# Kernel optimization log

Measured on AMD Instinct MI355X. Metric: run time of the kernel, lower is better.

Reference implementation:

```python
import jax, jax.numpy as jnp
import numpy as np

B, C, H, W = 16, 4, 512, 512


def setup_inputs() -> dict:
    key = jax.random.key(0)
    k_in, k_tg, k_mask = jax.random.split(key, 3)
    inp = jax.random.normal(k_in, (B, C, H, W), dtype=jnp.float32)
    tgt_vals = jax.random.normal(k_tg, (B, C, H, W), dtype=jnp.float32)
    mask = jax.random.randint(k_mask, (B, 1, H, W), 0, 2).astype(jnp.float32)
    target = jnp.concatenate([tgt_vals, mask], axis=1)  # [B, C+1, H, W]
    return {"input": inp, "target": target}


def reference(input, target):
    # mask = target[b, -1]; masked_select broadcasts mask over the C channels,
    # MSELoss means over the C*count selected elements; batches with empty
    # masks contribute 0; each batch contribution is divided by B.
    mask = (target[:, -1] == 1).astype(input.dtype)            # [B, H, W]
    diff2 = jnp.square(input - target[:, :-1])                 # [B, C, H, W]
    sum_b = jnp.einsum("bchw,bhw->b", diff2, mask)             # masked SSE per batch
    cnt_b = mask.sum(axis=(1, 2)) * input.shape[1]             # C * #masked pixels
    per_b = jnp.where(cnt_b > 0, sum_b / jnp.maximum(cnt_b, 1.0), 0.0)
    return per_b.sum() / input.shape[0]
```

## Files before the change

kernel.cpp:

```cpp
#include <hip/hip_runtime.h>


#define BATCH 16
#define CHAN 4
#define HWPIX (512 * 512)
#define BLOCKS_PER_BATCH 64
#define THREADS 256

__global__ __launch_bounds__(THREADS) void masked_mse_partial(
    const float* __restrict__ input,
    const float* __restrict__ target,
    float* __restrict__ ws) {
    const int b   = blockIdx.x / BLOCKS_PER_BATCH;
    const int blk = blockIdx.x % BLOCKS_PER_BATCH;

    const int groups           = HWPIX / 4;
    const int groups_per_block = groups / BLOCKS_PER_BATCH;

    const float* inb = input  + (size_t)b * CHAN * HWPIX;
    const float* tgb = target + (size_t)b * (CHAN + 1) * HWPIX;
    const float4* mask4 = (const float4*)(tgb + (size_t)CHAN * HWPIX);

    float s = 0.f, cnt = 0.f;

    const int g_end = (blk + 1) * groups_per_block;
    for (int g = blk * groups_per_block + threadIdx.x; g < g_end; g += THREADS) {
        float4 m = mask4[g];
        float mx = (m.x == 1.f) ? 1.f : 0.f;
        float my = (m.y == 1.f) ? 1.f : 0.f;
        float mz = (m.z == 1.f) ? 1.f : 0.f;
        float mw = (m.w == 1.f) ? 1.f : 0.f;
        cnt += mx + my + mz + mw;
#pragma unroll
        for (int c = 0; c < CHAN; ++c) {
            float4 a = ((const float4*)(inb + (size_t)c * HWPIX))[g];
            float4 t = ((const float4*)(tgb + (size_t)c * HWPIX))[g];
            float dx = a.x - t.x, dy = a.y - t.y, dz = a.z - t.z, dw = a.w - t.w;
            s += dx * dx * mx + dy * dy * my + dz * dz * mz + dw * dw * mw;
        }
    }

#pragma unroll
    for (int off = 32; off > 0; off >>= 1) {
        s   += __shfl_down(s, off, 64);
        cnt += __shfl_down(cnt, off, 64);
    }

    __shared__ float ss[THREADS / 64];
    __shared__ float sc[THREADS / 64];
    const int lane = threadIdx.x & 63;
    const int wid  = threadIdx.x >> 6;
    if (lane == 0) { ss[wid] = s; sc[wid] = cnt; }
    __syncthreads();

    if (threadIdx.x == 0) {
        float S = 0.f, Cn = 0.f;
#pragma unroll
        for (int w = 0; w < THREADS / 64; ++w) { S += ss[w]; Cn += sc[w]; }
        atomicAdd(&ws[2 * b],     S);
        atomicAdd(&ws[2 * b + 1], Cn);
    }
}

__global__ void masked_mse_final(const float* __restrict__ ws,
                                 float* __restrict__ out) {
    if (threadIdx.x == 0 && blockIdx.x == 0) {
        float acc = 0.f;
#pragma unroll
        for (int b = 0; b < BATCH; ++b) {
            float s  = ws[2 * b];
            float cb = ws[2 * b + 1] * (float)CHAN;
            acc += (cb > 0.f) ? (s / cb) : 0.f;
        }
        out[0] = acc / (float)BATCH;
    }
}

extern "C" void kernel_launch(void* const* d_in, const int* in_sizes, int n_in,
                              void* d_out, int out_size, void* d_ws, size_t ws_size,
                              hipStream_t stream) {
    const float* input  = (const float*)d_in[0];
    const float* target = (const float*)d_in[1];
    float* out = (float*)d_out;
    float* ws  = (float*)d_ws;

    hipMemsetAsync(ws, 0, 2 * BATCH * sizeof(float), stream);

    dim3 grid(BATCH * BLOCKS_PER_BATCH);
    dim3 block(THREADS);
    masked_mse_partial<<<grid, block, 0, stream>>>(input, target, ws);
    masked_mse_final<<<1, 64, 0, stream>>>(ws, out);
}
```

Baseline: 178.0 us.

## Fuse final reduction into partial kernel via last-block atomic counter

Removes the separate single-thread finalize kernel. Each block now bumps an atomic counter after publishing its partial sums, and the last block to finish computes the batch-averaged loss. This saves one kernel launch and its dependency gap, at the cost of a threadfence and atomic reads. The change also doubles the number of blocks per batch and unrolls the streaming loop by two to raise memory-level parallelism.

```diff
diff --git a/kernel.cpp b/kernel.cpp
--- a/kernel.cpp
+++ b/kernel.cpp
@@ -4,13 +4,17 @@
 #define BATCH 16
 #define CHAN 4
 #define HWPIX (512 * 512)
-#define BLOCKS_PER_BATCH 64
+#define BLOCKS_PER_BATCH 128
 #define THREADS 256
+#define TOTAL_BLOCKS (BATCH * BLOCKS_PER_BATCH)
 
-__global__ __launch_bounds__(THREADS) void masked_mse_partial(
+#define WS_FLOATS (2 * BATCH + 1)
+
+__global__ __launch_bounds__(THREADS) void masked_mse_fused(
     const float* __restrict__ input,
     const float* __restrict__ target,
-    float* __restrict__ ws) {
+    float* __restrict__ ws,
+    float* __restrict__ out) {
     const int b   = blockIdx.x / BLOCKS_PER_BATCH;
     const int blk = blockIdx.x % BLOCKS_PER_BATCH;
 
@@ -24,6 +28,7 @@
     float s = 0.f, cnt = 0.f;
 
     const int g_end = (blk + 1) * groups_per_block;
+#pragma unroll 2
     for (int g = blk * groups_per_block + threadIdx.x; g < g_end; g += THREADS) {
         float4 m = mask4[g];
         float mx = (m.x == 1.f) ? 1.f : 0.f;
@@ -59,20 +64,20 @@
         for (int w = 0; w < THREADS / 64; ++w) { S += ss[w]; Cn += sc[w]; }
         atomicAdd(&ws[2 * b],     S);
         atomicAdd(&ws[2 * b + 1], Cn);
-    }
-}
 
-__global__ void masked_mse_final(const float* __restrict__ ws,
-                                 float* __restrict__ out) {
-    if (threadIdx.x == 0 && blockIdx.x == 0) {
-        float acc = 0.f;
+        __threadfence();
+        unsigned int* counter = (unsigned int*)&ws[2 * BATCH];
+        unsigned int done = atomicAdd(counter, 1u);
+        if (done == TOTAL_BLOCKS - 1) {
+            float acc = 0.f;
 #pragma unroll
-        for (int b = 0; b < BATCH; ++b) {
-            float s  = ws[2 * b];
-            float cb = ws[2 * b + 1] * (float)CHAN;
-            acc += (cb > 0.f) ? (s / cb) : 0.f;
+            for (int bb = 0; bb < BATCH; ++bb) {
+                float sb = atomicAdd(&ws[2 * bb],     0.f);
+                float cb = atomicAdd(&ws[2 * bb + 1], 0.f) * (float)CHAN;
+                acc += (cb > 0.f) ? (sb / cb) : 0.f;
+            }
+            out[0] = acc / (float)BATCH;
         }
-        out[0] = acc / (float)BATCH;
     }
 }
 
@@ -84,10 +89,8 @@
     float* out = (float*)d_out;
     float* ws  = (float*)d_ws;
 
-    hipMemsetAsync(ws, 0, 2 * BATCH * sizeof(float), stream);
+    hipMemsetAsync(ws, 0, WS_FLOATS * sizeof(float), stream);
 
-    dim3 grid(BATCH * BLOCKS_PER_BATCH);
-    dim3 block(THREADS);
-    masked_mse_partial<<<grid, block, 0, stream>>>(input, target, ws);
-    masked_mse_final<<<1, 64, 0, stream>>>(ws, out);
+    masked_mse_fused<<<dim3(TOTAL_BLOCKS), dim3(THREADS), 0, stream>>>(
+        input, target, ws, out);
 }
```

Result: slower. 282.6 us (+58.8%).
